# Optimization experiments

Measured on AMD Instinct MI355X. Metric: run time of the kernel, lower is better.

## Reference

```python
import jax, jax.numpy as jnp
import numpy as np

EPS = 1e-5

def layernorm(x, w, b):
    mu = jnp.mean(x, axis=-1, keepdims=True)
    var = jnp.mean((x - mu) ** 2, axis=-1, keepdims=True)
    return (x - mu) / jnp.sqrt(var + EPS) * w + b

def setup_inputs() -> dict:
    key = jax.random.key(0)
    ks = jax.random.split(key, 20)
    N, E, G = 50000, 800000, 512
    IN, OUT, TXT, MAN = 128, 128, 768, 14
    d = {
        "x": jax.random.normal(ks[0], (N, IN), jnp.float32),
        "edge_index": jax.random.randint(ks[1], (2, E), 0, N),
        "batch": jnp.sort(jax.random.randint(ks[2], (N,), 0, G)),
        "batch_size": G,
        "text_embedding": jax.random.normal(ks[3], (G, TXT), jnp.float32),
        "features_embedding": jax.random.normal(ks[4], (G, MAN), jnp.float32),
        # params
        "ln_proj_w": jnp.ones((IN,)), "ln_proj_b": jnp.zeros((IN,)),
        "W_l": jax.random.normal(ks[5], (IN, OUT)) / np.sqrt(IN),
        "b_l": jnp.zeros((OUT,)),
        "W_r": jax.random.normal(ks[6], (IN, OUT)) / np.sqrt(IN),
        "ln_conv_w": jnp.ones((OUT,)), "ln_conv_b": jnp.zeros((OUT,)),
        "gate_w": jax.random.normal(ks[7], (OUT, 1)) / np.sqrt(OUT),
        "gate_b": jnp.zeros((1,)),
        "graph_weight": jnp.asarray(1.0, jnp.float32),
        "msg_W": jax.random.normal(ks[8], (TXT, OUT)) / np.sqrt(TXT),
        "msg_b": jnp.zeros((OUT,)),
        "feat_W": jax.random.normal(ks[9], (MAN, OUT)) / np.sqrt(MAN),
        "feat_b": jnp.zeros((OUT,)),
        "mixed_w": jnp.ones((3 * OUT,)), "mixed_b": jnp.zeros((3 * OUT,)),
        "fc1_W": jax.random.normal(ks[10], (3 * OUT, 1)) / np.sqrt(3 * OUT),
        "fc1_b": jnp.zeros((1,)),
    }
    return d

def reference(x, edge_index, batch, batch_size, text_embedding, features_embedding,
              ln_proj_w, ln_proj_b, W_l, b_l, W_r, ln_conv_w, ln_conv_b,
              gate_w, gate_b, graph_weight, msg_W, msg_b, feat_W, feat_b,
              mixed_w, mixed_b, fc1_W, fc1_b):
    N = x.shape[0]
    src, dst = edge_index[0], edge_index[1]
    # project_norm
    h = layernorm(x, ln_proj_w, ln_proj_b)
    # GraphSAGE (SAGEConv, mean aggregation): out = mean_j(h_j) @ W_l + b + h @ W_r
    msgs = h[src]                                   # [E, IN] gather
    agg = jax.ops.segment_sum(msgs, dst, num_segments=N)
    deg = jax.ops.segment_sum(jnp.ones((src.shape[0],), h.dtype), dst, num_segments=N)
    mean_nb = agg / jnp.maximum(deg, 1.0)[:, None]
    h = mean_nb @ W_l + b_l + h @ W_r
    # layernorm + gelu (HomogeneousGraphConvolution)
    h = jax.nn.gelu(layernorm(h, ln_conv_w, ln_conv_b), approximate=False)
    # AttentionalAggregation: scatter-softmax over `batch`
    gate = (h @ gate_w + gate_b)[:, 0]              # [N]
    seg_max = jax.ops.segment_max(gate, batch, num_segments=batch_size)
    seg_max = jnp.where(jnp.isfinite(seg_max), seg_max, 0.0)
    e = jnp.exp(gate - seg_max[batch])
    denom = jax.ops.segment_sum(e, batch, num_segments=batch_size)
    attn = (e / denom[batch])[:, None]              # [N,1]
    graph_embedding = jax.ops.segment_sum(attn * h, batch, num_segments=batch_size)
    # dropout is identity in eval mode
    weighted = graph_weight * graph_embedding
    msg_emb = jax.nn.gelu(text_embedding @ msg_W + msg_b, approximate=False)
    feat_emb = jax.nn.gelu(features_embedding @ feat_W + feat_b, approximate=False)
    emb = jnp.concatenate([weighted, msg_emb, feat_emb], axis=1)
    emb = layernorm(emb, mixed_w, mixed_b)
    logits = emb @ fc1_W + fc1_b
    return (logits, graph_embedding, attn)
```

## Files before the change

### kernel.cpp

```cpp
#include <hip/hip_runtime.h>


typedef unsigned short ushort_t;
typedef __attribute__((ext_vector_type(8))) short bf16x8;
typedef __attribute__((ext_vector_type(4))) float floatx4;

#define NBLK 128
#define MAXNB 1024

__device__ __forceinline__ float b2f(ushort_t u) {
    union { unsigned int i; float f; } v; v.i = ((unsigned int)u) << 16; return v.f;
}
__device__ __forceinline__ ushort_t f2b(float f) {
    union { float f; unsigned int i; } v; v.f = f;
    unsigned int x = v.i;
    return (ushort_t)((x + 0x7FFFu + ((x >> 16) & 1u)) >> 16);
}
__device__ __forceinline__ float gelu_f(float x) {
    return 0.5f * x * (1.0f + erff(x * 0.70710678118654752440f));
}
__device__ __forceinline__ float waveReduceSum(float v) {
#pragma unroll
    for (int o = 32; o; o >>= 1) v += __shfl_xor(v, o, 64);
    return v;
}
__device__ __forceinline__ float waveReduceMax(float v) {
#pragma unroll
    for (int o = 32; o; o >>= 1) v = fmaxf(v, __shfl_xor(v, o, 64));
    return v;
}

__global__ void k_prep(const float* __restrict__ Wl, const float* __restrict__ Wr,
                       ushort_t* __restrict__ Wt) {
    int id = blockIdx.x * 256 + threadIdx.x;
    if (id >= 32768) return;
    int n = id >> 8, k = id & 255;
    float v = (k < 128) ? Wl[k * 128 + n] : Wr[(k - 128) * 128 + n];
    Wt[n * 256 + k] = f2b(v);
}

__global__ void k_ln1(const float* __restrict__ x, const float* __restrict__ w,
                      const float* __restrict__ b, ushort_t* __restrict__ hb, int N) {
    int row  = (blockIdx.x * blockDim.x + threadIdx.x) >> 6;
    int lane = threadIdx.x & 63;
    if (row >= N) return;
    size_t base = (size_t)row * 128;
    float2 xv = ((const float2*)(x + base))[lane];
    float v0 = xv.x, v1 = xv.y;
    float s  = waveReduceSum(v0 + v1);
    float s2 = waveReduceSum(v0 * v0 + v1 * v1);
    float mu = s * (1.0f / 128.0f);
    float var = s2 * (1.0f / 128.0f) - mu * mu;
    float rstd = 1.0f / sqrtf(var + 1e-5f);
    int d = lane * 2;
    ushort2 ov;
    ov.x = f2b((v0 - mu) * rstd * w[d]     + b[d]);
    ov.y = f2b((v1 - mu) * rstd * w[d + 1] + b[d + 1]);
    ((ushort2*)(hb + base))[lane] = ov;
}

__global__ void k_deg(const int* __restrict__ ei, int* __restrict__ deg, int E) {
    int e = blockIdx.x * blockDim.x + threadIdx.x;
    if (e < E) atomicAdd(&deg[ei[E + e]], 1);
}

__global__ void k_chunksum(const int* __restrict__ deg, int* __restrict__ csum, int N) {
    int i = blockIdx.x * 256 + threadIdx.x;
    int v = (i < N) ? deg[i] : 0;
#pragma unroll
    for (int o = 32; o; o >>= 1) v += __shfl_xor(v, o, 64);
    __shared__ int buf[4];
    int lane = threadIdx.x & 63, wv = threadIdx.x >> 6;
    if (lane == 0) buf[wv] = v;
    __syncthreads();
    if (threadIdx.x == 0) csum[blockIdx.x] = buf[0] + buf[1] + buf[2] + buf[3];
}
__global__ void k_chunkscan(const int* __restrict__ csum, int* __restrict__ coff, int nch) {
    int t = threadIdx.x;
    int v = (t < nch) ? csum[t] : 0;
    __shared__ int sb[256];
    sb[t] = v; __syncthreads();
    for (int o = 1; o < 256; o <<= 1) {
        int a = (t >= o) ? sb[t - o] : 0;
        __syncthreads();
        sb[t] += a;
        __syncthreads();
    }
    coff[t] = sb[t] - v;
}
__global__ void k_cursor(const int* __restrict__ deg, const int* __restrict__ coff,
                         int* __restrict__ cursor, int N) {
    int t = threadIdx.x;
    int i = blockIdx.x * 256 + t;
    int v = (i < N) ? deg[i] : 0;
    __shared__ int sb[256];
    sb[t] = v; __syncthreads();
    for (int o = 1; o < 256; o <<= 1) {
        int a = (t >= o) ? sb[t - o] : 0;
        __syncthreads();
        sb[t] += a;
        __syncthreads();
    }
    if (i < N) cursor[i] = sb[t] - v + coff[blockIdx.x];
}

__global__ void __launch_bounds__(256) k_hist(
    const int* __restrict__ ei, int* __restrict__ bhist, int E, int nb, int chunk) {
    __shared__ int hist[MAXNB];
    int blk = blockIdx.x, t = threadIdx.x;
    for (int i = t; i < nb; i += 256) hist[i] = 0;
    __syncthreads();
    int e0 = blk * chunk, e1 = min(e0 + chunk, E);
    for (int e = e0 + t; e < e1; e += 256)
        atomicAdd(&hist[ei[E + e] >> 7], 1);
    __syncthreads();
    for (int i = t; i < nb; i += 256) bhist[i * NBLK + blk] = hist[i];
}

__global__ void __launch_bounds__(256) k_bscan(
    const int* __restrict__ bhist, const int* __restrict__ cursor,
    int* __restrict__ boff, int nb) {
    int t = threadIdx.x;
    for (int b = t; b < nb; b += 256) {
        int run = cursor[b << 7];
        const int* row = bhist + b * NBLK;
#pragma unroll 8
        for (int blk = 0; blk < NBLK; blk++) {
            boff[blk * nb + b] = run;
            run += row[blk];
        }
    }
}

__global__ void __launch_bounds__(256) k_bplace(
    const int* __restrict__ ei, const int* __restrict__ boff,
    unsigned int* __restrict__ packed, int E, int nb, int chunk) {
    __shared__ int lcur[MAXNB];
    int blk = blockIdx.x, t = threadIdx.x;
    for (int i = t; i < nb; i += 256) lcur[i] = boff[blk * nb + i];
    __syncthreads();
    int e0 = blk * chunk, e1 = min(e0 + chunk, E);
    for (int e = e0 + t; e < e1; e += 256) {
        int s = ei[e], d = ei[E + e];
        int pos = atomicAdd(&lcur[d >> 7], 1);
        packed[pos] = ((unsigned int)(d & 127) << 25) | (unsigned int)s;
    }
}

__global__ void __launch_bounds__(256) k_bsort(
    const unsigned int* __restrict__ packed, const int* __restrict__ cursor,
    int* __restrict__ nbr, int N, int E) {
    __shared__ int lcur[128];
    int b = blockIdx.x, t = threadIdx.x;
    int node0 = b << 7;
    if (t < 128) {
        int node = node0 + t;
        lcur[t] = (node < N) ? cursor[node] : 0;
    }
    __syncthreads();
    int gstart = cursor[node0];
    int next = node0 + 128;
    int gend = (next < N) ? cursor[next] : E;
    for (int i = gstart + t; i < gend; i += 256) {
        unsigned int p = packed[i];
        int pos = atomicAdd(&lcur[p >> 25], 1);
        nbr[pos] = (int)(p & 0x1FFFFFFu);
    }
}

__global__ void k_aggcsr(const ushort_t* __restrict__ hb, const int* __restrict__ cursor,
                         const int* __restrict__ deg, const int* __restrict__ nbr,
                         ushort_t* __restrict__ meanb, int N) {
    int node = (blockIdx.x * blockDim.x + threadIdx.x) >> 6;
    int lane = threadIdx.x & 63;
    if (node >= N) return;
    int dg = deg[node];
    int st = cursor[node];
    float a0 = 0.f, a1 = 0.f;
    int j = 0;
    for (; j + 4 <= dg; j += 4) {
        int s0 = nbr[st + j],     s1 = nbr[st + j + 1];
        int s2 = nbr[st + j + 2], s3 = nbr[st + j + 3];
        ushort2 v0 = ((const ushort2*)(hb + (size_t)s0 * 128))[lane];
        ushort2 v1 = ((const ushort2*)(hb + (size_t)s1 * 128))[lane];
        ushort2 v2 = ((const ushort2*)(hb + (size_t)s2 * 128))[lane];
        ushort2 v3 = ((const ushort2*)(hb + (size_t)s3 * 128))[lane];
        a0 += b2f(v0.x) + b2f(v1.x) + b2f(v2.x) + b2f(v3.x);
        a1 += b2f(v0.y) + b2f(v1.y) + b2f(v2.y) + b2f(v3.y);
    }
    for (; j < dg; j++) {
        int s = nbr[st + j];
        ushort2 v = ((const ushort2*)(hb + (size_t)s * 128))[lane];
        a0 += b2f(v.x); a1 += b2f(v.y);
    }
    float inv = 1.0f / fmaxf((float)dg, 1.0f);
    ushort2 ov; ov.x = f2b(a0 * inv); ov.y = f2b(a1 * inv);
    ((ushort2*)(meanb + (size_t)node * 128))[lane] = ov;
}

__global__ void __launch_bounds__(256) k_gemm(
    const ushort_t* __restrict__ meanb, ushort_t* __restrict__ hb,
    const ushort_t* __restrict__ Wt, const float* __restrict__ bl,
    const float* __restrict__ lnw, const float* __restrict__ lnb,
    const float* __restrict__ gw, const float* __restrict__ gb,
    float* __restrict__ gate, int N) {
    __shared__ ushort_t A[16][264];
    __shared__ float H2[16][132];
    int t = threadIdx.x;
    int row0 = blockIdx.x * 16;
    {
        int r = t >> 4, i = t & 15;
        int row = row0 + r; if (row >= N) row = N - 1;
        *(bf16x8*)&A[r][i * 8]       = *(const bf16x8*)(meanb + (size_t)row * 128 + i * 8);
        *(bf16x8*)&A[r][128 + i * 8] = *(const bf16x8*)(hb    + (size_t)row * 128 + i * 8);
    }
    __syncthreads();
    int w = t >> 6, l = t & 63;
    int m16 = l & 15, quad = l >> 4;
    int n0 = w * 32 + m16;
    int n1 = n0 + 16;
    floatx4 acc0 = {0.f, 0.f, 0.f, 0.f}, acc1 = {0.f, 0.f, 0.f, 0.f};
    for (int ks = 0; ks < 256; ks += 32) {
        bf16x8 a  = *(const bf16x8*)&A[m16][ks + quad * 8];
        bf16x8 b0 = *(const bf16x8*)(Wt + (size_t)n0 * 256 + ks + quad * 8);
        bf16x8 b1 = *(const bf16x8*)(Wt + (size_t)n1 * 256 + ks + quad * 8);
        acc0 = __builtin_amdgcn_mfma_f32_16x16x32_bf16(a, b0, acc0, 0, 0, 0);
        acc1 = __builtin_amdgcn_mfma_f32_16x16x32_bf16(a, b1, acc1, 0, 0, 0);
    }
#pragma unroll
    for (int i = 0; i < 4; i++) {
        H2[quad * 4 + i][n0] = acc0[i];
        H2[quad * 4 + i][n1] = acc1[i];
    }
    __syncthreads();
    int d = l * 2;
    float bb0 = bl[d],  bb1 = bl[d + 1];
    float lw0 = lnw[d], lw1 = lnw[d + 1];
    float lb0 = lnb[d], lb1 = lnb[d + 1];
    float gw0 = gw[d],  gw1 = gw[d + 1];
    float gbias = gb[0];
#pragma unroll
    for (int rr = 0; rr < 4; rr++) {
        int r = w * 4 + rr;
        int row = row0 + r;
        if (row >= N) break;
        float v0 = H2[r][d] + bb0, v1 = H2[r][d + 1] + bb1;
        float s  = waveReduceSum(v0 + v1);
        float s2 = waveReduceSum(v0 * v0 + v1 * v1);
        float mu = s * (1.f / 128.f);
        float var = s2 * (1.f / 128.f) - mu * mu;
        float rstd = 1.0f / sqrtf(var + 1e-5f);
        float g0 = gelu_f((v0 - mu) * rstd * lw0 + lb0);
        float g1 = gelu_f((v1 - mu) * rstd * lw1 + lb1);
        float gp = waveReduceSum(g0 * gw0 + g1 * gw1);
        ushort2 ov; ov.x = f2b(g0); ov.y = f2b(g1);
        ((ushort2*)(hb + (size_t)row * 128))[l] = ov;
        if (l == 0) gate[row] = gp + gbias;
    }
}

__global__ void k_segstart(const int* __restrict__ batch, int* __restrict__ segstart,
                           int N, int G) {
    int i = blockIdx.x * blockDim.x + threadIdx.x;
    if (i >= N) return;
    int b = batch[i];
    if (i == 0) {
        for (int g = 0; g <= b; g++) segstart[g] = 0;
    } else {
        int pb = batch[i - 1];
        for (int g = pb + 1; g <= b; g++) segstart[g] = i;
    }
    if (i == N - 1) {
        for (int g = b + 1; g <= G; g++) segstart[g] = N;
    }
}

__global__ void __launch_bounds__(128) k_attn(
    const float* __restrict__ gate, const ushort_t* __restrict__ h3b,
    const int* __restrict__ segstart,
    float* __restrict__ ge_out, float* __restrict__ attn_out, int G) {
    int g = blockIdx.x, t = threadIdx.x;
    int s0 = segstart[g], s1 = segstart[g + 1];
    if (s1 <= s0) {
        ge_out[(size_t)g * 128 + t] = 0.0f;
        return;
    }
    int lane = t & 63, wv = t >> 6;
    __shared__ float wbuf[2];
    __shared__ float pbuf[128];
    float m = -3.0e38f;
    for (int i = s0 + t; i < s1; i += 128) m = fmaxf(m, gate[i]);
    m = waveReduceMax(m);
    if (lane == 0) wbuf[wv] = m;
    __syncthreads();
    m = fmaxf(wbuf[0], wbuf[1]);
    __syncthreads();
    float dsum = 0.f;
    for (int i = s0 + t; i < s1; i += 128) dsum += expf(gate[i] - m);
    dsum = waveReduceSum(dsum);
    if (lane == 0) wbuf[wv] = dsum;
    __syncthreads();
    float inv = 1.0f / (wbuf[0] + wbuf[1]);
    float acc = 0.f;
    for (int base = s0; base < s1; base += 128) {
        int n = min(128, s1 - base);
        __syncthreads();
        if (t < n) {
            float p = expf(gate[base + t] - m) * inv;
            pbuf[t] = p;
            attn_out[base + t] = p;
        }
        __syncthreads();
        for (int j = 0; j < n; j++)
            acc += pbuf[j] * b2f(h3b[(size_t)(base + j) * 128 + t]);
    }
    ge_out[(size_t)g * 128 + t] = acc;
}

__global__ void __launch_bounds__(128) k_tail(
    const float* __restrict__ text, const float* __restrict__ feats,
    const float* __restrict__ msgW, const float* __restrict__ msgb,
    const float* __restrict__ featW, const float* __restrict__ featb,
    const float* __restrict__ gwt, const float* __restrict__ mixw,
    const float* __restrict__ mixb, const float* __restrict__ fc1W,
    const float* __restrict__ fc1b, const float* __restrict__ ge,
    float* __restrict__ logits, int G) {
    int g = blockIdx.x, t = threadIdx.x;
    __shared__ float txt[768];
    __shared__ float rbuf[4];
    for (int i = t; i < 768; i += 128) txt[i] = text[(size_t)g * 768 + i];
    __syncthreads();
    float am = msgb[t];
    for (int k = 0; k < 768; k += 4) {
        float4 a = *(const float4*)&txt[k];
        am += a.x * msgW[(k + 0) * 128 + t] + a.y * msgW[(k + 1) * 128 + t]
            + a.z * msgW[(k + 2) * 128 + t] + a.w * msgW[(k + 3) * 128 + t];
    }
    float me = gelu_f(am);
    float af = featb[t];
#pragma unroll
    for (int k = 0; k < 14; k++) af += feats[g * 14 + k] * featW[k * 128 + t];
    float fe = gelu_f(af);
    float e0 = gwt[0] * ge[(size_t)g * 128 + t];
    float ps = e0 + me + fe, ps2 = e0 * e0 + me * me + fe * fe;
    int lane = t & 63, w = t >> 6;
    float r1 = waveReduceSum(ps), r2 = waveReduceSum(ps2);
    if (lane == 0) { rbuf[w] = r1; rbuf[2 + w] = r2; }
    __syncthreads();
    float S = rbuf[0] + rbuf[1], S2 = rbuf[2] + rbuf[3];
    float mu = S * (1.f / 384.f);
    float var = S2 * (1.f / 384.f) - mu * mu;
    float rstd = 1.0f / sqrtf(var + 1e-5f);
    float n0 = (e0 - mu) * rstd * mixw[t]       + mixb[t];
    float n1 = (me - mu) * rstd * mixw[128 + t] + mixb[128 + t];
    float n2 = (fe - mu) * rstd * mixw[256 + t] + mixb[256 + t];
    float lp = n0 * fc1W[t] + n1 * fc1W[128 + t] + n2 * fc1W[256 + t];
    __syncthreads();
    float r3 = waveReduceSum(lp);
    if (lane == 0) rbuf[w] = r3;
    __syncthreads();
    if (t == 0) logits[g] = rbuf[0] + rbuf[1] + fc1b[0];
}

extern "C" void kernel_launch(void* const* d_in, const int* in_sizes, int n_in,
                              void* d_out, int out_size, void* d_ws, size_t ws_size,
                              hipStream_t stream) {
    const float* x     = (const float*)d_in[0];
    const int*   ei    = (const int*)d_in[1];
    const int*   batch = (const int*)d_in[2];
    const float* text  = (const float*)d_in[4];
    const float* feats = (const float*)d_in[5];
    const float* lnpw  = (const float*)d_in[6];
    const float* lnpb  = (const float*)d_in[7];
    const float* Wl    = (const float*)d_in[8];
    const float* bl    = (const float*)d_in[9];
    const float* Wr    = (const float*)d_in[10];
    const float* lncw  = (const float*)d_in[11];
    const float* lncb  = (const float*)d_in[12];
    const float* gatew = (const float*)d_in[13];
    const float* gateb = (const float*)d_in[14];
    const float* gwt   = (const float*)d_in[15];
    const float* msgW  = (const float*)d_in[16];
    const float* msgb  = (const float*)d_in[17];
    const float* featW = (const float*)d_in[18];
    const float* featb = (const float*)d_in[19];
    const float* mixw  = (const float*)d_in[20];
    const float* mixb  = (const float*)d_in[21];
    const float* fc1W  = (const float*)d_in[22];
    const float* fc1b  = (const float*)d_in[23];

    int N = in_sizes[0] / 128;
    int E = in_sizes[1] / 2;
    int G = in_sizes[4] / 768;

    char* wp = (char*)d_ws;
    auto alloc = [&](size_t bytes) -> char* {
        char* p = wp; wp += (bytes + 255) & ~(size_t)255; return p;
    };
    ushort_t* hb     = (ushort_t*)alloc((size_t)N * 128 * 2);
    ushort_t* meanb  = (ushort_t*)alloc((size_t)N * 128 * 2);
    ushort_t* Wt     = (ushort_t*)alloc(128 * 256 * 2);
    float*    gate   = (float*)alloc((size_t)N * 4);
    int*      deg    = (int*)alloc((size_t)N * 4);
    int*      cursor = (int*)alloc((size_t)N * 4);
    int*      nbr    = (int*)alloc((size_t)E * 4);
    unsigned int* packed = (unsigned int*)alloc((size_t)E * 4);
    int*      csum   = (int*)alloc(1024 * 4);
    int*      coff   = (int*)alloc(1024 * 4);
    int*      segst  = (int*)alloc((size_t)(G + 2) * 4);

    int nch = (N + 255) / 256;
    int nb  = (N + 127) / 128;
    int chunk = (E + NBLK - 1) / NBLK;

    int* bhist = (int*)alloc((size_t)nb * NBLK * 4);
    int* boff  = (int*)alloc((size_t)NBLK * nb * 4);

    float* logits_out = (float*)d_out;
    float* ge_out     = logits_out + G;
    float* attn_out   = ge_out + (size_t)G * 128;

    hipMemsetAsync(deg, 0, (size_t)N * 4, stream);

    k_prep     <<<128,               256, 0, stream>>>(Wl, Wr, Wt);
    k_ln1      <<<(N + 3) / 4,       256, 0, stream>>>(x, lnpw, lnpb, hb, N);
    k_deg      <<<(E + 255) / 256,   256, 0, stream>>>(ei, deg, E);
    k_chunksum <<<nch,               256, 0, stream>>>(deg, csum, N);
    k_chunkscan<<<1,                 256, 0, stream>>>(csum, coff, nch);
    k_cursor   <<<nch,               256, 0, stream>>>(deg, coff, cursor, N);
    k_hist     <<<NBLK,              256, 0, stream>>>(ei, bhist, E, nb, chunk);
    k_bscan    <<<1,                 256, 0, stream>>>(bhist, cursor, boff, nb);
    k_bplace   <<<NBLK,              256, 0, stream>>>(ei, boff, packed, E, nb, chunk);
    k_bsort    <<<nb,                256, 0, stream>>>(packed, cursor, nbr, N, E);
    k_aggcsr   <<<(N + 3) / 4,       256, 0, stream>>>(hb, cursor, deg, nbr, meanb, N);
    k_gemm     <<<(N + 15) / 16,     256, 0, stream>>>(meanb, hb, Wt, bl, lncw, lncb,
                                                       gatew, gateb, gate, N);
    k_segstart <<<(N + 255) / 256,   256, 0, stream>>>(batch, segst, N, G);
    k_attn     <<<G,                 128, 0, stream>>>(gate, hb, segst, ge_out, attn_out, G);
    k_tail     <<<G,                 128, 0, stream>>>(text, feats, msgW, msgb, featW, featb,
                                                       gwt, mixw, mixb, fc1W, fc1b,
                                                       ge_out, logits_out, G);
}
```

Measured before the change: 310.7 us.

## Fuse degree/histogram, attention/tail kernels; binary-search segments; unroll aggregation by 8

Merges the degree-count and bucket-histogram passes into one kernel so the edge destination array is read once. Replaces the segment-start kernel with a per-block binary search over the sorted batch array and fuses attention pooling with the tail MLP/layernorm, so the graph embedding never round-trips through global memory. The neighbour aggregation loop also gets an 8-wide unrolled stage for more loads in flight. Together these cut three kernel launches. In exchange, the fused degree/histogram kernel now issues its global atomics from only 128 blocks, which may lower parallelism for that step.

```diff
diff --git a/kernel.cpp b/kernel.cpp
--- a/kernel.cpp
+++ b/kernel.cpp
@@ -28,6 +28,11 @@
 #pragma unroll
     for (int o = 32; o; o >>= 1) v = fmaxf(v, __shfl_xor(v, o, 64));
     return v;
+}
+__device__ __forceinline__ int lowerBound(const int* __restrict__ a, int n, int v) {
+    int lo = 0, hi = n;
+    while (lo < hi) { int mid = (lo + hi) >> 1; if (a[mid] < v) lo = mid + 1; else hi = mid; }
+    return lo;
 }
 
 __global__ void k_prep(const float* __restrict__ Wl, const float* __restrict__ Wr,
@@ -59,9 +64,21 @@
     ((ushort2*)(hb + base))[lane] = ov;
 }
 
-__global__ void k_deg(const int* __restrict__ ei, int* __restrict__ deg, int E) {
-    int e = blockIdx.x * blockDim.x + threadIdx.x;
-    if (e < E) atomicAdd(&deg[ei[E + e]], 1);
+__global__ void __launch_bounds__(256) k_deghist(
+    const int* __restrict__ ei, int* __restrict__ deg, int* __restrict__ bhist,
+    int E, int nb, int chunk) {
+    __shared__ int hist[MAXNB];
+    int blk = blockIdx.x, t = threadIdx.x;
+    for (int i = t; i < nb; i += 256) hist[i] = 0;
+    __syncthreads();
+    int e0 = blk * chunk, e1 = min(e0 + chunk, E);
+    for (int e = e0 + t; e < e1; e += 256) {
+        int d = ei[E + e];
+        atomicAdd(&deg[d], 1);
+        atomicAdd(&hist[d >> 7], 1);
+    }
+    __syncthreads();
+    for (int i = t; i < nb; i += 256) bhist[i * NBLK + blk] = hist[i];
 }
 
 __global__ void k_chunksum(const int* __restrict__ deg, int* __restrict__ csum, int N) {
@@ -102,19 +119,6 @@
         __syncthreads();
     }
     if (i < N) cursor[i] = sb[t] - v + coff[blockIdx.x];
-}
-
-__global__ void __launch_bounds__(256) k_hist(
-    const int* __restrict__ ei, int* __restrict__ bhist, int E, int nb, int chunk) {
-    __shared__ int hist[MAXNB];
-    int blk = blockIdx.x, t = threadIdx.x;
-    for (int i = t; i < nb; i += 256) hist[i] = 0;
-    __syncthreads();
-    int e0 = blk * chunk, e1 = min(e0 + chunk, E);
-    for (int e = e0 + t; e < e1; e += 256)
-        atomicAdd(&hist[ei[E + e] >> 7], 1);
-    __syncthreads();
-    for (int i = t; i < nb; i += 256) bhist[i * NBLK + blk] = hist[i];
 }
 
 __global__ void __launch_bounds__(256) k_bscan(
@@ -178,6 +182,24 @@
     int st = cursor[node];
     float a0 = 0.f, a1 = 0.f;
     int j = 0;
+    for (; j + 8 <= dg; j += 8) {
+        int s0 = nbr[st + j],     s1 = nbr[st + j + 1];
+        int s2 = nbr[st + j + 2], s3 = nbr[st + j + 3];
+        int s4 = nbr[st + j + 4], s5 = nbr[st + j + 5];
+        int s6 = nbr[st + j + 6], s7 = nbr[st + j + 7];
+        ushort2 v0 = ((const ushort2*)(hb + (size_t)s0 * 128))[lane];
+        ushort2 v1 = ((const ushort2*)(hb + (size_t)s1 * 128))[lane];
+        ushort2 v2 = ((const ushort2*)(hb + (size_t)s2 * 128))[lane];
+        ushort2 v3 = ((const ushort2*)(hb + (size_t)s3 * 128))[lane];
+        ushort2 v4 = ((const ushort2*)(hb + (size_t)s4 * 128))[lane];
+        ushort2 v5 = ((const ushort2*)(hb + (size_t)s5 * 128))[lane];
+        ushort2 v6 = ((const ushort2*)(hb + (size_t)s6 * 128))[lane];
+        ushort2 v7 = ((const ushort2*)(hb + (size_t)s7 * 128))[lane];
+        a0 += b2f(v0.x) + b2f(v1.x) + b2f(v2.x) + b2f(v3.x)
+            + b2f(v4.x) + b2f(v5.x) + b2f(v6.x) + b2f(v7.x);
+        a1 += b2f(v0.y) + b2f(v1.y) + b2f(v2.y) + b2f(v3.y)
+            + b2f(v4.y) + b2f(v5.y) + b2f(v6.y) + b2f(v7.y);
+    }
     for (; j + 4 <= dg; j += 4) {
         int s0 = nbr[st + j],     s1 = nbr[st + j + 1];
         int s2 = nbr[st + j + 2], s3 = nbr[st + j + 3];
@@ -259,77 +281,57 @@
     }
 }
 
-__global__ void k_segstart(const int* __restrict__ batch, int* __restrict__ segstart,
-                           int N, int G) {
-    int i = blockIdx.x * blockDim.x + threadIdx.x;
-    if (i >= N) return;
-    int b = batch[i];
-    if (i == 0) {
-        for (int g = 0; g <= b; g++) segstart[g] = 0;
-    } else {
-        int pb = batch[i - 1];
-        for (int g = pb + 1; g <= b; g++) segstart[g] = i;
-    }
-    if (i == N - 1) {
-        for (int g = b + 1; g <= G; g++) segstart[g] = N;
-    }
-}
-
-__global__ void __launch_bounds__(128) k_attn(
+__global__ void __launch_bounds__(128) k_attntail(
     const float* __restrict__ gate, const ushort_t* __restrict__ h3b,
-    const int* __restrict__ segstart,
-    float* __restrict__ ge_out, float* __restrict__ attn_out, int G) {
-    int g = blockIdx.x, t = threadIdx.x;
-    int s0 = segstart[g], s1 = segstart[g + 1];
-    if (s1 <= s0) {
-        ge_out[(size_t)g * 128 + t] = 0.0f;
-        return;
-    }
-    int lane = t & 63, wv = t >> 6;
-    __shared__ float wbuf[2];
-    __shared__ float pbuf[128];
-    float m = -3.0e38f;
-    for (int i = s0 + t; i < s1; i += 128) m = fmaxf(m, gate[i]);
-    m = waveReduceMax(m);
-    if (lane == 0) wbuf[wv] = m;
-    __syncthreads();
-    m = fmaxf(wbuf[0], wbuf[1]);
-    __syncthreads();
-    float dsum = 0.f;
-    for (int i = s0 + t; i < s1; i += 128) dsum += expf(gate[i] - m);
-    dsum = waveReduceSum(dsum);
-    if (lane == 0) wbuf[wv] = dsum;
-    __syncthreads();
-    float inv = 1.0f / (wbuf[0] + wbuf[1]);
-    float acc = 0.f;
-    for (int base = s0; base < s1; base += 128) {
-        int n = min(128, s1 - base);
-        __syncthreads();
-        if (t < n) {
-            float p = expf(gate[base + t] - m) * inv;
-            pbuf[t] = p;
-            attn_out[base + t] = p;
-        }
-        __syncthreads();
-        for (int j = 0; j < n; j++)
-            acc += pbuf[j] * b2f(h3b[(size_t)(base + j) * 128 + t]);
-    }
-    ge_out[(size_t)g * 128 + t] = acc;
-}
-
-__global__ void __launch_bounds__(128) k_tail(
+    const int* __restrict__ batch,
     const float* __restrict__ text, const float* __restrict__ feats,
     const float* __restrict__ msgW, const float* __restrict__ msgb,
     const float* __restrict__ featW, const float* __restrict__ featb,
     const float* __restrict__ gwt, const float* __restrict__ mixw,
     const float* __restrict__ mixb, const float* __restrict__ fc1W,
-    const float* __restrict__ fc1b, const float* __restrict__ ge,
-    float* __restrict__ logits, int G) {
+    const float* __restrict__ fc1b,
+    float* __restrict__ ge_out, float* __restrict__ attn_out,
+    float* __restrict__ logits, int N, int G) {
     int g = blockIdx.x, t = threadIdx.x;
+    __shared__ int sbound[2];
+    __shared__ float wbuf[2];
+    __shared__ float pbuf[128];
     __shared__ float txt[768];
     __shared__ float rbuf[4];
+    if (t < 2) sbound[t] = lowerBound(batch, N, g + t);
     for (int i = t; i < 768; i += 128) txt[i] = text[(size_t)g * 768 + i];
     __syncthreads();
+    int s0 = sbound[0], s1 = sbound[1];
+    int lane = t & 63, wv = t >> 6;
+    float acc = 0.f;
+    if (s1 > s0) {
+        float m = -3.0e38f;
+        for (int i = s0 + t; i < s1; i += 128) m = fmaxf(m, gate[i]);
+        m = waveReduceMax(m);
+        if (lane == 0) wbuf[wv] = m;
+        __syncthreads();
+        m = fmaxf(wbuf[0], wbuf[1]);
+        __syncthreads();
+        float dsum = 0.f;
+        for (int i = s0 + t; i < s1; i += 128) dsum += expf(gate[i] - m);
+        dsum = waveReduceSum(dsum);
+        if (lane == 0) wbuf[wv] = dsum;
+        __syncthreads();
+        float inv = 1.0f / (wbuf[0] + wbuf[1]);
+        for (int base = s0; base < s1; base += 128) {
+            int n = min(128, s1 - base);
+            __syncthreads();
+            if (t < n) {
+                float p = expf(gate[base + t] - m) * inv;
+                pbuf[t] = p;
+                attn_out[base + t] = p;
+            }
+            __syncthreads();
+            for (int j = 0; j < n; j++)
+                acc += pbuf[j] * b2f(h3b[(size_t)(base + j) * 128 + t]);
+        }
+    }
+    ge_out[(size_t)g * 128 + t] = acc;
     float am = msgb[t];
     for (int k = 0; k < 768; k += 4) {
         float4 a = *(const float4*)&txt[k];
@@ -341,11 +343,11 @@
 #pragma unroll
     for (int k = 0; k < 14; k++) af += feats[g * 14 + k] * featW[k * 128 + t];
     float fe = gelu_f(af);
-    float e0 = gwt[0] * ge[(size_t)g * 128 + t];
+    float e0 = gwt[0] * acc;
     float ps = e0 + me + fe, ps2 = e0 * e0 + me * me + fe * fe;
-    int lane = t & 63, w = t >> 6;
     float r1 = waveReduceSum(ps), r2 = waveReduceSum(ps2);
-    if (lane == 0) { rbuf[w] = r1; rbuf[2 + w] = r2; }
+    __syncthreads();
+    if (lane == 0) { rbuf[wv] = r1; rbuf[2 + wv] = r2; }
     __syncthreads();
     float S = rbuf[0] + rbuf[1], S2 = rbuf[2] + rbuf[3];
     float mu = S * (1.f / 384.f);
@@ -355,9 +357,9 @@
     float n1 = (me - mu) * rstd * mixw[128 + t] + mixb[128 + t];
     float n2 = (fe - mu) * rstd * mixw[256 + t] + mixb[256 + t];
     float lp = n0 * fc1W[t] + n1 * fc1W[128 + t] + n2 * fc1W[256 + t];
-    __syncthreads();
     float r3 = waveReduceSum(lp);
-    if (lane == 0) rbuf[w] = r3;
+    __syncthreads();
+    if (lane == 0) rbuf[wv] = r3;
     __syncthreads();
     if (t == 0) logits[g] = rbuf[0] + rbuf[1] + fc1b[0];
 }
@@ -407,7 +409,6 @@
     unsigned int* packed = (unsigned int*)alloc((size_t)E * 4);
     int*      csum   = (int*)alloc(1024 * 4);
     int*      coff   = (int*)alloc(1024 * 4);
-    int*      segst  = (int*)alloc((size_t)(G + 2) * 4);
 
     int nch = (N + 255) / 256;
     int nb  = (N + 127) / 128;
@@ -424,20 +425,18 @@
 
     k_prep     <<<128,               256, 0, stream>>>(Wl, Wr, Wt);
     k_ln1      <<<(N + 3) / 4,       256, 0, stream>>>(x, lnpw, lnpb, hb, N);
-    k_deg      <<<(E + 255) / 256,   256, 0, stream>>>(ei, deg, E);
+    k_deghist  <<<NBLK,              256, 0, stream>>>(ei, deg, bhist, E, nb, chunk);
     k_chunksum <<<nch,               256, 0, stream>>>(deg, csum, N);
     k_chunkscan<<<1,                 256, 0, stream>>>(csum, coff, nch);
     k_cursor   <<<nch,               256, 0, stream>>>(deg, coff, cursor, N);
-    k_hist     <<<NBLK,              256, 0, stream>>>(ei, bhist, E, nb, chunk);
     k_bscan    <<<1,                 256, 0, stream>>>(bhist, cursor, boff, nb);
     k_bplace   <<<NBLK,              256, 0, stream>>>(ei, boff, packed, E, nb, chunk);
     k_bsort    <<<nb,                256, 0, stream>>>(packed, cursor, nbr, N, E);
     k_aggcsr   <<<(N + 3) / 4,       256, 0, stream>>>(hb, cursor, deg, nbr, meanb, N);
     k_gemm     <<<(N + 15) / 16,     256, 0, stream>>>(meanb, hb, Wt, bl, lncw, lncb,
                                                        gatew, gateb, gate, N);
-    k_segstart <<<(N + 255) / 256,   256, 0, stream>>>(batch, segst, N, G);
-    k_attn     <<<G,                 128, 0, stream>>>(gate, hb, segst, ge_out, attn_out, G);
-    k_tail     <<<G,                 128, 0, stream>>>(text, feats, msgW, msgb, featW, featb,
-                                                       gwt, mixw, mixb, fc1W, fc1b,
-                                                       ge_out, logits_out, G);
-}
+    k_attntail <<<G,                 128, 0, stream>>>(gate, hb, batch, text, feats,
+                                                       msgW, msgb, featW, featb, gwt,
+                                                       mixw, mixb, fc1W, fc1b,
+                                                       ge_out, attn_out, logits_out, N, G);
+}
```

After: 294.7 us. 1.05x faster.
